# Kernel tuning notes

Measured on AMD Instinct MI355X. Metric: run time of the kernel, lower is better.

Reference implementation:

```python
import jax, jax.numpy as jnp
import numpy as np

T = 1024
B = 32768


def _rbf_kan(x, grid, spline_w, base_w):
    # x: [N, in], grid: [G], spline_w: [in*G, out], base_w: [out, in]
    base = x @ base_w.T  # [N, out]
    diff = x[:, :, None] - grid[None, None, :]  # [N, in, G]
    basis = jnp.exp(-(diff * diff) * 10.0).reshape(x.shape[0], -1)  # [N, in*G]
    return base + basis @ spline_w


def setup_inputs() -> dict:
    key = jax.random.key(0)
    ks = jax.random.split(key, 6)
    t_steps = (jnp.arange(T, dtype=jnp.float32) / T).reshape(T, 1)  # uniform grid, dt = 1/T
    initial_I = jax.random.uniform(ks[0], (B,), dtype=jnp.float32)
    grid1 = jnp.linspace(0.0, 1.0, 50, dtype=jnp.float32)
    spline_w1 = jax.random.normal(ks[1], (1 * 50, 32), dtype=jnp.float32) * 0.1 + 0.2
    base_w1 = jax.random.normal(ks[2], (32, 1), dtype=jnp.float32) * 0.1 + 0.2
    grid2 = jnp.linspace(0.0, 1.0, 20, dtype=jnp.float32)
    spline_w2 = jax.random.normal(ks[3], (32 * 20, 1), dtype=jnp.float32) * 0.1 + 0.2
    base_w2 = jax.random.normal(ks[4], (1, 32), dtype=jnp.float32) * 0.1 + 0.2
    gamma_param = jnp.array([5.0], dtype=jnp.float32)
    return {"t_steps": t_steps, "initial_I": initial_I,
            "grid1": grid1, "spline_w1": spline_w1, "base_w1": base_w1,
            "grid2": grid2, "spline_w2": spline_w2, "base_w2": base_w2,
            "gamma_param": gamma_param}


def reference(t_steps, initial_I, grid1, spline_w1, base_w1, grid2, spline_w2, base_w2, gamma_param):
    # beta(t) via 2-layer RBF-KAN, softplus-positive
    h = _rbf_kan(t_steps, grid1, spline_w1, base_w1)        # [T, 32]
    betas = jax.nn.softplus(_rbf_kan(h, grid2, spline_w2, base_w2))  # [T, 1]
    gamma = jax.nn.softplus(gamma_param)                    # [1]
    dt = t_steps[1] - t_steps[0]                            # [1]

    I0 = initial_I                                          # [B]
    S0 = 1.0 - I0

    def step(carry, beta):
        I, S = carry
        new_inf = beta * S * I
        dI = new_inf - gamma * I
        I2 = jnp.clip(I + dt * dI, 0.0, 5.0)
        S2 = jnp.clip(S - dt * new_inf, 0.0, 5.0)
        return (I2, S2), I2

    _, sim_I = jax.lax.scan(step, (I0, S0), betas)          # sim_I: [T, B]
    return sim_I
```

## Files before the change

### kernel.cpp

```cpp
#include <hip/hip_runtime.h>
#include <cstddef>

#define T_STEPS 1024
#define BATCH   32768
#define G1      50
#define H1      32
#define G2      20

__device__ __forceinline__ float softplus_f(float x) {
    float e = __expf(-fabsf(x));
    return fmaxf(x, 0.0f) + __logf(1.0f + e);
}

__global__ __launch_bounds__(64) void beta_kernel(
    const float* __restrict__ t_steps,
    const float* __restrict__ grid1,
    const float* __restrict__ spline_w1,
    const float* __restrict__ base_w1,
    const float* __restrict__ grid2,
    const float* __restrict__ spline_w2,
    const float* __restrict__ base_w2,
    float* __restrict__ a_out)
{
    __shared__ float se[G1];
    __shared__ float sh[H1];

    const int t    = blockIdx.x;
    const int lane = threadIdx.x;
    const float x  = t_steps[t];

    if (lane < G1) {
        float d = x - grid1[lane];
        se[lane] = __expf(-10.0f * d * d);
    }
    __syncthreads();

    if (lane < H1) {
        float acc = x * base_w1[lane];
        #pragma unroll
        for (int g = 0; g < G1; ++g)
            acc = fmaf(se[g], spline_w1[g * H1 + lane], acc);
        sh[lane] = acc;
    }
    __syncthreads();

    float acc = 0.0f;
    #pragma unroll
    for (int k = 0; k < 10; ++k) {
        int p = lane + 64 * k;
        int j = p / G2;
        int g = p - j * G2;
        float d = sh[j] - grid2[g];
        acc = fmaf(__expf(-10.0f * d * d), spline_w2[p], acc);
    }
    if (lane < H1) acc = fmaf(sh[lane], base_w2[lane], acc);

    #pragma unroll
    for (int ofs = 32; ofs >= 1; ofs >>= 1)
        acc += __shfl_xor(acc, ofs, 64);

    if (lane == 0) {
        float dt = t_steps[1] - t_steps[0];
        a_out[t] = dt * softplus_f(acc);
    }
}

__global__ __launch_bounds__(128) void scan_kernel(
    const float* __restrict__ t_steps,
    const float* __restrict__ initial_I,
    const float* __restrict__ gamma_param,
    const float* __restrict__ a_in,
    float* __restrict__ out)
{
    __shared__ float4 sa4[T_STEPS / 4];
    {
        const float4* g4 = (const float4*)a_in;
        #pragma unroll
        for (int i = 0; i < T_STEPS / 4 / 128; ++i)
            sa4[threadIdx.x + i * 128] = g4[threadIdx.x + i * 128];
    }
    __syncthreads();

    const int b = blockIdx.x * 128 + threadIdx.x;
    float I = initial_I[b];
    float S = 1.0f - I;
    const float gamma = softplus_f(gamma_param[0]);
    const float dt = t_steps[1] - t_steps[0];
    const float c = fmaf(-dt, gamma, 1.0f);
    float* outp = out + b;

    #pragma unroll 1
    for (int tb = 0; tb < T_STEPS; tb += 16) {
        float4 q[4];
        #pragma unroll
        for (int k = 0; k < 4; ++k) q[k] = sa4[tb / 4 + k];
        const float* av = (const float*)q;
        #pragma unroll
        for (int k = 0; k < 16; ++k) {
            float a  = av[k];
            float f  = fmaf(a, S, c);
            float u  = fmaf(-a, I, 1.0f);
            float In = I * f;
            float Sn = S * u;
            I = fminf(fmaxf(In, 0.0f), 5.0f);
            S = fminf(fmaxf(Sn, 0.0f), 5.0f);
            outp[(size_t)(tb + k) * BATCH] = I;
        }
    }
}

extern "C" void kernel_launch(void* const* d_in, const int* in_sizes, int n_in,
                              void* d_out, int out_size, void* d_ws, size_t ws_size,
                              hipStream_t stream) {
    const float* t_steps     = (const float*)d_in[0];
    const float* initial_I   = (const float*)d_in[1];
    const float* grid1       = (const float*)d_in[2];
    const float* spline_w1   = (const float*)d_in[3];
    const float* base_w1     = (const float*)d_in[4];
    const float* grid2       = (const float*)d_in[5];
    const float* spline_w2   = (const float*)d_in[6];
    const float* base_w2     = (const float*)d_in[7];
    const float* gamma_param = (const float*)d_in[8];
    float* out = (float*)d_out;
    float* a_t = (float*)d_ws;

    beta_kernel<<<T_STEPS, 64, 0, stream>>>(
        t_steps, grid1, spline_w1, base_w1, grid2, spline_w2, base_w2, a_t);
    scan_kernel<<<BATCH / 128, 128, 0, stream>>>(
        t_steps, initial_I, gamma_param, a_t, out);
}
```

Baseline: 158.4 us.

## Split scan into checkpoint prepass and segmented parallel replay

A prepass kernel runs the recurrence without storing outputs and records I and S at the start of each of 8 time segments. A replay kernel then launches one block row per segment, so 8 times as many blocks recompute their segment and write the outputs. The aim is more parallelism and more concurrent memory traffic for the output writes, which were limited to only 256 blocks. The cost is roughly twice the recurrence arithmetic plus an extra launch and checkpoint traffic.

```diff
diff --git a/kernel.cpp b/kernel.cpp
--- a/kernel.cpp
+++ b/kernel.cpp
@@ -6,6 +6,8 @@
 #define G1      50
 #define H1      32
 #define G2      20
+#define NSEG    8
+#define SEGLEN  (T_STEPS / NSEG)
 
 __device__ __forceinline__ float softplus_f(float x) {
     float e = __expf(-fabsf(x));
@@ -65,12 +67,12 @@
     }
 }
 
-__global__ __launch_bounds__(128) void scan_kernel(
+__global__ __launch_bounds__(128) void prepass_kernel(
     const float* __restrict__ t_steps,
     const float* __restrict__ initial_I,
     const float* __restrict__ gamma_param,
     const float* __restrict__ a_in,
-    float* __restrict__ out)
+    float* __restrict__ ck)
 {
     __shared__ float4 sa4[T_STEPS / 4];
     {
@@ -87,13 +89,65 @@
     const float gamma = softplus_f(gamma_param[0]);
     const float dt = t_steps[1] - t_steps[0];
     const float c = fmaf(-dt, gamma, 1.0f);
-    float* outp = out + b;
 
     #pragma unroll 1
-    for (int tb = 0; tb < T_STEPS; tb += 16) {
+    for (int s = 0; s < NSEG - 1; ++s) {
+        #pragma unroll 1
+        for (int tb = s * SEGLEN; tb < (s + 1) * SEGLEN; tb += 16) {
+            float4 q[4];
+            #pragma unroll
+            for (int k = 0; k < 4; ++k) q[k] = sa4[tb / 4 + k];
+            const float* av = (const float*)q;
+            #pragma unroll
+            for (int k = 0; k < 16; ++k) {
+                float a  = av[k];
+                float f  = fmaf(a, S, c);
+                float u  = fmaf(-a, I, 1.0f);
+                float In = I * f;
+                float Sn = S * u;
+                I = fminf(fmaxf(In, 0.0f), 5.0f);
+                S = fminf(fmaxf(Sn, 0.0f), 5.0f);
+            }
+        }
+        ck[(size_t)s * BATCH + b]                      = I;
+        ck[(size_t)(NSEG - 1 + s) * BATCH + b]         = S;
+    }
+}
+
+__global__ __launch_bounds__(128) void replay_kernel(
+    const float* __restrict__ t_steps,
+    const float* __restrict__ initial_I,
+    const float* __restrict__ gamma_param,
+    const float* __restrict__ a_in,
+    const float* __restrict__ ck,
+    float* __restrict__ out)
+{
+    __shared__ float sa[SEGLEN];
+    const int s   = blockIdx.y;
+    const int tid = threadIdx.x;
+    sa[tid] = a_in[s * SEGLEN + tid];
+    __syncthreads();
+
+    const int b = blockIdx.x * 128 + tid;
+    float I, S;
+    if (s == 0) {
+        I = initial_I[b];
+        S = 1.0f - I;
+    } else {
+        I = ck[(size_t)(s - 1) * BATCH + b];
+        S = ck[(size_t)(NSEG - 1 + s - 1) * BATCH + b];
+    }
+    const float gamma = softplus_f(gamma_param[0]);
+    const float dt = t_steps[1] - t_steps[0];
+    const float c = fmaf(-dt, gamma, 1.0f);
+
+    float* outp = out + (size_t)s * SEGLEN * BATCH + b;
+
+    #pragma unroll 1
+    for (int tb = 0; tb < SEGLEN; tb += 16) {
         float4 q[4];
         #pragma unroll
-        for (int k = 0; k < 4; ++k) q[k] = sa4[tb / 4 + k];
+        for (int k = 0; k < 4; ++k) q[k] = ((const float4*)sa)[tb / 4 + k];
         const float* av = (const float*)q;
         #pragma unroll
         for (int k = 0; k < 16; ++k) {
@@ -123,9 +177,13 @@
     const float* gamma_param = (const float*)d_in[8];
     float* out = (float*)d_out;
     float* a_t = (float*)d_ws;
+    float* ck  = (float*)((char*)d_ws + 4096);
 
     beta_kernel<<<T_STEPS, 64, 0, stream>>>(
         t_steps, grid1, spline_w1, base_w1, grid2, spline_w2, base_w2, a_t);
-    scan_kernel<<<BATCH / 128, 128, 0, stream>>>(
-        t_steps, initial_I, gamma_param, a_t, out);
+    prepass_kernel<<<BATCH / 128, 128, 0, stream>>>(
+        t_steps, initial_I, gamma_param, a_t, ck);
+    dim3 grid(BATCH / 128, NSEG);
+    replay_kernel<<<grid, 128, 0, stream>>>(
+        t_steps, initial_I, gamma_param, a_t, ck, out);
 }
```

After: 170.9 us. +7.9%, slower.
